# Performance work log

Hardware: AMD Instinct MI355X
Metric: run time of the kernel (lower is better)

Reference implementation:

```python
import jax, jax.numpy as jnp
import numpy as np
from jax import lax

# ---- fixed configuration (matches init_kwargs / input_specs) ----
L, E, V, F, HU, HL, S = 32, 1024, 2048, 8, 128, 2, 7
D0, D1R, D1E = 512, 129, 640
D = S + 1                      # path dimension = num_slices + 1
SIGLEN = D + D * D + D * D * D # iisignature.siglength(8, 3) = 584
FINAL = F * 2 * SIGLEN         # 9344
EPS = 1e-5                     # BatchNorm eps


def _bn(x, g, b):
    # BatchNorm1d in training mode: biased batch statistics over axis 0
    mu = x.mean(0)
    var = x.var(0)
    return (x - mu) / jnp.sqrt(var + EPS) * g + b


def _mlp(x, Win, bin_, gin, betain, Wh, bh, gh, betah, Wout, bout, gout, betaout):
    # eigf: Linear+BN+ReLU blocks, 1 -> HU -> ... -> HU -> 1
    h = jax.nn.relu(_bn(x @ Win.T + bin_, gin, betain))
    for l in range(HL):
        h = jax.nn.relu(_bn(h @ Wh[l].T + bh[l], gh[l], betah[l]))
    o = jax.nn.relu(_bn(h @ Wout.T + bout, gout, betaout))
    return o[:, 0]


# ---- path signature, level 3, via Chen's identity (replaces iisignature.sig) ----
def _seg(dx):
    s1 = dx
    s2 = jnp.outer(s1, dx).reshape(-1) * 0.5
    s3 = jnp.outer(s2, dx).reshape(-1) / 3.0
    return (s1, s2, s3)


def _chen(Sg, T):
    s1, s2, s3 = Sg
    t1, t2, t3 = T
    r1 = s1 + t1
    r2 = s2 + t2 + jnp.outer(s1, t1).reshape(-1)
    r3 = s3 + t3 + jnp.outer(s1, t2).reshape(-1) + jnp.outer(s2, t1).reshape(-1)
    return (r1, r2, r3)


def _sig3(path):  # path [P, D] -> [SIGLEN]
    dX = path[1:] - path[:-1]

    def step(Sg, dx):
        return _chen(Sg, _seg(dx)), None

    Sg, _ = lax.scan(step, _seg(dX[0]), dX[1:])
    return jnp.concatenate(Sg)


def _diagram_sig(vals, W_proj, b_proj):
    # Conv1d(1, S, kernel=2, stride=2) == pairwise projection; then sort, prepend time axis
    pairs = vals.reshape(-1, 2)                      # [P, 2]
    P = pairs.shape[0]
    proj = jnp.einsum('pk,sk->sp', pairs, W_proj[:, 0, :]) + b_proj[:, None]  # [S, P]
    proj = jnp.sort(proj, axis=-1)
    t = jnp.arange(P, dtype=vals.dtype) / (P * (P + 1) / 2.0)
    path = jnp.concatenate([t[None, :], proj], axis=0).T  # [P, D]
    return _sig3(path)


def setup_inputs() -> dict:
    key = jax.random.key(0)
    ks = iter(jax.random.split(key, 16))
    nrm = lambda kk, shp, sc: jax.random.normal(kk, shp, jnp.float32) * sc
    inp = {
        "eigenvalues": jax.random.uniform(next(ks), (L, E), jnp.float32),
        "eigenvectors_sq": jax.random.uniform(next(ks), (L, E, V), jnp.float32) / E,
        "dgm0": jax.random.randint(next(ks), (L, F, D0), 0, V, jnp.int32),
        "dgm1rel": jax.random.randint(next(ks), (L, F, D1R), 0, V, jnp.int32),
        "dgm1ext": jax.random.randint(next(ks), (L, F, D1E), 0, V, jnp.int32),
        "mlp_Win": nrm(next(ks), (F, HU, 1), 1.0),
        "mlp_bin": jnp.zeros((F, HU), jnp.float32),
        "mlp_gin": jnp.ones((F, HU), jnp.float32),
        "mlp_betain": jnp.zeros((F, HU), jnp.float32),
        "mlp_Wh": nrm(next(ks), (F, HL, HU, HU), 1.0 / np.sqrt(HU)),
        "mlp_bh": jnp.zeros((F, HL, HU), jnp.float32),
        "mlp_gh": jnp.ones((F, HL, HU), jnp.float32),
        "mlp_betah": jnp.zeros((F, HL, HU), jnp.float32),
        "mlp_Wout": nrm(next(ks), (F, 1, HU), 1.0 / np.sqrt(HU)),
        "mlp_bout": jnp.zeros((F, 1), jnp.float32),
        "mlp_gout": jnp.ones((F, 1), jnp.float32),
        "mlp_betaout": jnp.zeros((F, 1), jnp.float32),
        "W_proj": nrm(next(ks), (S, 1, 2), 0.7),
        "b_proj": jnp.zeros((S,), jnp.float32),
        "W_fin": nrm(next(ks), (1, FINAL), 1.0 / np.sqrt(FINAL)),
        "b_fin": jnp.zeros((1,), jnp.float32),
        "g_fin": jnp.ones((1,), jnp.float32),
        "beta_fin": jnp.zeros((1,), jnp.float32),
    }
    return inp


def reference(eigenvalues, eigenvectors_sq, dgm0, dgm1rel, dgm1ext,
              mlp_Win, mlp_bin, mlp_gin, mlp_betain,
              mlp_Wh, mlp_bh, mlp_gh, mlp_betah,
              mlp_Wout, mlp_bout, mlp_gout, mlp_betaout,
              W_proj, b_proj, W_fin, b_fin, g_fin, beta_fin):
    flat = eigenvalues.reshape(-1, 1)  # [L*E, 1], sample-major like the torch flatten
    evs = jax.vmap(lambda *p: _mlp(flat, *p))(
        mlp_Win, mlp_bin, mlp_gin, mlp_betain,
        mlp_Wh, mlp_bh, mlp_gh, mlp_betah,
        mlp_Wout, mlp_bout, mlp_gout, mlp_betaout)  # [F, L*E]
    # per-sample filtration values: evs_transformed[:, slice_i] @ eigvecsq_i
    f = jnp.einsum('fle,lev->lfv', evs.reshape(F, L, E), eigenvectors_sq)  # [L, F, V]
    fv = f.reshape(L * F, V)
    d0 = jnp.take_along_axis(fv, dgm0.reshape(L * F, D0), axis=1)
    rel = jnp.take_along_axis(fv, dgm1rel.reshape(L * F, D1R), axis=1)
    # torch.arange(len-1, 0, -1): reversed, dropping element 0
    Dgm0 = jnp.concatenate([d0, rel[:, 1:][:, ::-1]], axis=1)  # [L*F, 640]
    Dgm1 = jnp.take_along_axis(fv, dgm1ext.reshape(L * F, D1E), axis=1)
    sig0 = jax.vmap(lambda v: _diagram_sig(v, W_proj, b_proj))(Dgm0)  # [L*F, SIGLEN]
    sig1 = jax.vmap(lambda v: _diagram_sig(v, W_proj, b_proj))(Dgm1)
    x = jnp.concatenate([sig0, sig1], axis=-1).reshape(L, FINAL)
    out = x @ W_fin.T + b_fin  # dropout p=0.0 -> identity
    return _bn(out, g_fin, beta_fin)  # [L, 1]
```

## Files before the change

kernel.cpp:

```cpp
#include <hip/hip_runtime.h>
#include <cfloat>
#include <math.h>

#define N_SAMP 32768
#define FF 8
#define HU 128
#define LL 32
#define EE 1024
#define VV 2048
#define PP 320
#define SIGLEN 584
#define FINAL_W 9344

__device__ __forceinline__ int frag_pos(int m) {
  return ((m & 4) << 4) | ((m >> 3) << 2) | (m & 3);
}

__device__ __forceinline__ double wave_red(double v) {
#pragma unroll
  for (int off = 32; off > 0; off >>= 1) v += __shfl_xor(v, off, 64);
  return v;
}

__global__ __launch_bounds__(256) void k_xstats(const float* __restrict__ x,
                                                double* __restrict__ xst) {
  const int tid = threadIdx.x;
  double s1 = 0.0, s2 = 0.0;
  for (int i = tid; i < N_SAMP; i += 256) { double v = (double)x[i]; s1 += v; s2 += v * v; }
  __shared__ double r1[4], r2[4];
  double w1 = wave_red(s1), w2 = wave_red(s2);
  int wave = tid >> 6, lane = tid & 63;
  if (lane == 0) { r1[wave] = w1; r2[wave] = w2; }
  __syncthreads();
  if (tid == 0) {
    xst[0] = r1[0] + r1[1] + r1[2] + r1[3];
    xst[1] = r2[0] + r2[1] + r2[2] + r2[3];
  }
}

template<int MODE>
__global__ __launch_bounds__(256, 4)
void k_gemm(const float* __restrict__ Ain,
            const double* __restrict__ xstats,
            const float* __restrict__ w_in,
            const float* __restrict__ g_in,
            const float* __restrict__ beta_in,
            const float* __restrict__ sc,
            const float* __restrict__ sh,
            const float* __restrict__ Wb, int wstride,
            const float* __restrict__ bb, int bstride,
            float* __restrict__ Yt_out,
            double* __restrict__ stats) {
  __shared__ __align__(16) float As[32][132];
  __shared__ __align__(16) float Bs[32][132];
  __shared__ __align__(16) float p0[HU], p1[HU], biasl[HU], xl[HU];
  const int tid = threadIdx.x;
  const int f = blockIdx.y;
  const int m0 = blockIdx.x * 128;

  if (tid < HU) {
    biasl[tid] = bb[(size_t)f * bstride + tid];
    if (MODE == 0) {
      double mx = xstats[0] * (1.0 / 32768.0);
      double vx = xstats[1] * (1.0 / 32768.0) - mx * mx;
      if (vx < 0) vx = 0;
      float w = w_in[f * HU + tid];
      double inv = 1.0 / sqrt((double)w * (double)w * vx + 1e-5);
      float sj = (float)inv * g_in[f * HU + tid] * w;
      p0[tid] = sj;
      p1[tid] = beta_in[f * HU + tid] - (float)mx * sj;
      xl[tid] = Ain[m0 + tid];
    } else {
      p0[tid] = sc[f * HU + tid];
      p1[tid] = sh[f * HU + tid];
    }
  }

  float cacc[8][8];
#pragma unroll
  for (int i = 0; i < 8; ++i)
#pragma unroll
    for (int j = 0; j < 8; ++j) cacc[i][j] = 0.f;

  const int tidm = tid & 15, tidn = tid >> 4;

  for (int kk = 0; kk < 128; kk += 32) {
    __syncthreads();
#pragma unroll
    for (int r = 0; r < 4; ++r) {
      int flat4 = tid + r * 256;
      int k = flat4 >> 5;
      int mc = flat4 & 31;
      int pos = ((mc & 1) << 6) | ((mc >> 1) << 2);
      float a0, a1, a2, a3;
      if (MODE == 0) {
        const float4 xv = *(const float4*)&xl[mc * 4];
        float s = p0[kk + k], t = p1[kk + k];
        a0 = fmaxf(fmaf(xv.x, s, t), 0.f);
        a1 = fmaxf(fmaf(xv.y, s, t), 0.f);
        a2 = fmaxf(fmaf(xv.z, s, t), 0.f);
        a3 = fmaxf(fmaf(xv.w, s, t), 0.f);
      } else {
        const float4 yv = *(const float4*)(Ain + ((size_t)(f * HU + kk + k)) * N_SAMP + m0 + mc * 4);
        float s = p0[kk + k], t = p1[kk + k];
        a0 = fmaxf(fmaf(yv.x, s, t), 0.f);
        a1 = fmaxf(fmaf(yv.y, s, t), 0.f);
        a2 = fmaxf(fmaf(yv.z, s, t), 0.f);
        a3 = fmaxf(fmaf(yv.w, s, t), 0.f);
      }
      *(float4*)&As[k][pos] = make_float4(a0, a1, a2, a3);
    }
#pragma unroll
    for (int r = 0; r < 4; ++r) {
      int flat = tid + r * 256;
      int n = flat >> 3, kf = flat & 7;
      const float4 wv = *(const float4*)(Wb + (size_t)f * wstride + n * HU + kk + kf * 4);
      int pn = frag_pos(n);
      Bs[kf * 4 + 0][pn] = wv.x;
      Bs[kf * 4 + 1][pn] = wv.y;
      Bs[kf * 4 + 2][pn] = wv.z;
      Bs[kf * 4 + 3][pn] = wv.w;
    }
    __syncthreads();
#pragma unroll
    for (int k = 0; k < 32; ++k) {
      float4 a0 = *(const float4*)&As[k][tidm * 4];
      float4 a1 = *(const float4*)&As[k][64 + tidm * 4];
      float4 b0 = *(const float4*)&Bs[k][tidn * 4];
      float4 b1 = *(const float4*)&Bs[k][64 + tidn * 4];
      float av[8] = {a0.x, a0.y, a0.z, a0.w, a1.x, a1.y, a1.z, a1.w};
      float bv[8] = {b0.x, b0.y, b0.z, b0.w, b1.x, b1.y, b1.z, b1.w};
#pragma unroll
      for (int i = 0; i < 8; ++i)
#pragma unroll
        for (int j = 0; j < 8; ++j) cacc[i][j] = fmaf(av[i], bv[j], cacc[i][j]);
    }
  }
  __syncthreads();

  float cs1[8], cs2[8];
#pragma unroll
  for (int j = 0; j < 8; ++j) { cs1[j] = 0.f; cs2[j] = 0.f; }
#pragma unroll
  for (int jj = 0; jj < 8; ++jj) {
    int j = tidn * 8 + jj;
    float b = biasl[j];
    float o[8];
#pragma unroll
    for (int i = 0; i < 8; ++i) {
      float v = cacc[i][jj] + b;
      o[i] = v;
      cs1[jj] += v;
      cs2[jj] = fmaf(v, v, cs2[jj]);
    }
    float* dst = Yt_out + ((size_t)(f * HU + j)) * N_SAMP + m0 + tidm * 8;
    *(float4*)dst = make_float4(o[0], o[1], o[2], o[3]);
    *(float4*)(dst + 4) = make_float4(o[4], o[5], o[6], o[7]);
  }
  float* red1 = &As[0][0];
  float* red2 = &Bs[0][0];
#pragma unroll
  for (int j = 0; j < 8; ++j) red1[tidm * 128 + tidn * 8 + j] = cs1[j];
#pragma unroll
  for (int j = 0; j < 8; ++j) red2[tidm * 128 + tidn * 8 + j] = cs2[j];
  __syncthreads();
  {
    int which = tid >> 7, n = tid & 127;
    const float* rp = which ? red2 : red1;
    float s = 0.f;
#pragma unroll
    for (int r = 0; r < 16; ++r) s += rp[r * 128 + n];
    atomicAdd(&stats[(f * HU + n) * 2 + which], (double)s);
  }
}

__global__ __launch_bounds__(256) void k_fin(const double* __restrict__ stats,
                                             const float* __restrict__ g,
                                             const float* __restrict__ beta,
                                             int per_f, int gstride, int count,
                                             float* __restrict__ sc, float* __restrict__ sh) {
  int idx = blockIdx.x * 256 + threadIdx.x;
  if (idx >= count) return;
  int f = idx / per_f, j = idx - f * per_f;
  double S1 = stats[idx * 2 + 0], S2 = stats[idx * 2 + 1];
  double mean = S1 * (1.0 / 32768.0);
  double var = S2 * (1.0 / 32768.0) - mean * mean;
  if (var < 0) var = 0;
  double inv = 1.0 / sqrt(var + 1e-5);
  float gg = g[f * gstride + j];
  float scv = (float)inv * gg;
  sc[idx] = scv;
  sh[idx] = beta[f * gstride + j] - (float)mean * scv;
}

__global__ __launch_bounds__(256, 4) void k_outlayer(const float* __restrict__ Yt,
                                                     const float* __restrict__ sc2,
                                                     const float* __restrict__ sh2,
                                                     const float* __restrict__ Wout,
                                                     const float* __restrict__ bout,
                                                     float* __restrict__ evs_pre,
                                                     double* __restrict__ stats3) {
  __shared__ float wj[HU], scl[HU], shl[HU];
  const int tid = threadIdx.x;
  const int f = blockIdx.y;
  const int i = blockIdx.x * 256 + tid;
  if (tid < HU) {
    wj[tid] = Wout[f * HU + tid];
    scl[tid] = sc2[f * HU + tid];
    shl[tid] = sh2[f * HU + tid];
  }
  __syncthreads();
  const float* base = Yt + (size_t)f * HU * N_SAMP + i;
  float acc = 0.f;
#pragma unroll
  for (int j = 0; j < HU; ++j) {
    float y = base[(size_t)j * N_SAMP];
    acc = fmaf(fmaxf(fmaf(y, scl[j], shl[j]), 0.f), wj[j], acc);
  }
  float yo = acc + bout[f];
  evs_pre[(size_t)f * N_SAMP + i] = yo;
  double v = (double)yo;
  double s1 = wave_red(v), s2 = wave_red(v * v);
  __shared__ double r1[4], r2[4];
  int wave = tid >> 6, lane = tid & 63;
  if (lane == 0) { r1[wave] = s1; r2[wave] = s2; }
  __syncthreads();
  if (tid == 0) atomicAdd(&stats3[f * 2 + 0], r1[0] + r1[1] + r1[2] + r1[3]);
  if (tid == 1) atomicAdd(&stats3[f * 2 + 1], r2[0] + r2[1] + r2[2] + r2[3]);
}

__global__ __launch_bounds__(256) void k_einsum(const float* __restrict__ evs_pre,
                                                const float* __restrict__ sc3,
                                                const float* __restrict__ sh3,
                                                const float* __restrict__ eig,
                                                float* __restrict__ fv) {
  __shared__ float ev[FF * EE];
  const int tid = threadIdx.x;
  const int l = blockIdx.y;
  const int v0 = blockIdx.x * 256;
#pragma unroll
  for (int r = 0; r < 32; ++r) {
    int q = tid + r * 256;
    int f = q >> 10, e = q & 1023;
    float y = evs_pre[(size_t)f * N_SAMP + l * EE + e];
    ev[q] = fmaxf(fmaf(y, sc3[f], sh3[f]), 0.f);
  }
  __syncthreads();
  const float* up = eig + (size_t)l * EE * VV + v0 + tid;
  float acc[8] = {0, 0, 0, 0, 0, 0, 0, 0};
  for (int e0 = 0; e0 < EE; e0 += 32) {
    float u[32];
#pragma unroll
    for (int t = 0; t < 32; ++t) u[t] = up[(size_t)(e0 + t) * VV];
#pragma unroll
    for (int t = 0; t < 32; ++t) {
#pragma unroll
      for (int f = 0; f < 8; ++f) acc[f] = fmaf(ev[f * EE + e0 + t], u[t], acc[f]);
    }
  }
#pragma unroll
  for (int f = 0; f < 8; ++f) fv[((size_t)(l * FF + f)) * VV + v0 + tid] = acc[f];
}

__global__ __launch_bounds__(256) void k_diagram(const float* __restrict__ fv,
                                                 const int* __restrict__ dgm0,
                                                 const int* __restrict__ dgm1rel,
                                                 const int* __restrict__ dgm1ext,
                                                 const float* __restrict__ Wp,
                                                 const float* __restrict__ bp,
                                                 float* __restrict__ xbuf) {
  __shared__ float vals[640];
  __shared__ float ps[7 * 512];
  __shared__ float dXl[320][8];
  const int tid = threadIdx.x;
  const int bid = blockIdx.x;
  const int row = bid >> 1;
  const int c = bid & 1;
  const float* fvr = fv + (size_t)row * VV;

  for (int k = tid; k < 640; k += 256) {
    int idx;
    if (c == 0) idx = (k < 512) ? dgm0[(size_t)row * 512 + k] : dgm1rel[(size_t)row * 129 + (640 - k)];
    else        idx = dgm1ext[(size_t)row * 640 + k];
    vals[k] = fvr[idx];
  }
  __syncthreads();
  for (int q = tid; q < 7 * 512; q += 256) {
    int s = q >> 9, p = q & 511;
    float pv = 3.402823466e+38f;
    if (p < PP) pv = fmaf(Wp[2 * s + 1], vals[2 * p + 1], fmaf(Wp[2 * s], vals[2 * p], bp[s]));
    ps[s * 512 + p] = pv;
  }
  for (int k = 2; k <= 512; k <<= 1) {
    for (int j = k >> 1; j > 0; j >>= 1) {
      __syncthreads();
      for (int q = tid; q < 1792; q += 256) {
        int s = q >> 8, ip = q & 255;
        int i = ((ip & ~(j - 1)) << 1) | (ip & (j - 1));
        int p2 = i | j;
        float a = ps[s * 512 + i], b = ps[s * 512 + p2];
        bool up = ((i & k) == 0);
        if ((a > b) == up) { ps[s * 512 + i] = b; ps[s * 512 + p2] = a; }
      }
    }
  }
  __syncthreads();
  for (int q = tid; q < 319 * 8; q += 256) {
    int p = q >> 3, d = q & 7;
    dXl[p][d] = (d == 0) ? (1.0f / 51360.0f)
                         : ps[(d - 1) * 512 + p + 1] - ps[(d - 1) * 512 + p];
  }
  __syncthreads();
  if (tid < 64) {
    const int a = tid >> 3, b = tid & 7;
    float s1a = 0.f, s2r = 0.f;
    float s3r[8] = {0, 0, 0, 0, 0, 0, 0, 0};
    for (int p = 0; p < 319; ++p) {
      float4 dlo = *(const float4*)&dXl[p][0];
      float4 dhi = *(const float4*)&dXl[p][4];
      float dxa = dXl[p][a];
      float dxb = dXl[p][b];
      float coefA = fmaf(dxa, (1.f / 3.f), s1a);
      float w = fmaf(0.5f * dxb, coefA, s2r);
      s2r = fmaf(dxb, fmaf(0.5f, dxa, s1a), s2r);
      s3r[0] = fmaf(w, dlo.x, s3r[0]);
      s3r[1] = fmaf(w, dlo.y, s3r[1]);
      s3r[2] = fmaf(w, dlo.z, s3r[2]);
      s3r[3] = fmaf(w, dlo.w, s3r[3]);
      s3r[4] = fmaf(w, dhi.x, s3r[4]);
      s3r[5] = fmaf(w, dhi.y, s3r[5]);
      s3r[6] = fmaf(w, dhi.z, s3r[6]);
      s3r[7] = fmaf(w, dhi.w, s3r[7]);
      s1a += dxa;
    }
    const int l = row >> 3, ff = row & 7;
    float* xr = xbuf + (size_t)l * FINAL_W + ff * (2 * SIGLEN) + c * SIGLEN;
    if ((tid & 7) == 0) xr[a] = s1a;
    xr[8 + tid] = s2r;
    float* s3p = xr + 72 + tid * 8;
    *(float4*)(s3p + 0) = make_float4(s3r[0], s3r[1], s3r[2], s3r[3]);
    *(float4*)(s3p + 4) = make_float4(s3r[4], s3r[5], s3r[6], s3r[7]);
  }
}

__global__ __launch_bounds__(256) void k_rowdot(const float* __restrict__ xbuf,
                                                const float* __restrict__ Wf,
                                                const float* __restrict__ bf,
                                                double* __restrict__ outpre) {
  const int tid = threadIdx.x, l = blockIdx.x;
  const float* xr = xbuf + (size_t)l * FINAL_W;
  double acc = 0.0;
  for (int k = tid; k < FINAL_W; k += 256) acc += (double)xr[k] * (double)Wf[k];
  acc = wave_red(acc);
  __shared__ double r[4];
  int wave = tid >> 6, lane = tid & 63;
  if (lane == 0) r[wave] = acc;
  __syncthreads();
  if (tid == 0) outpre[l] = r[0] + r[1] + r[2] + r[3] + (double)bf[0];
}

__global__ __launch_bounds__(64) void k_bnfin(const double* __restrict__ outpre,
                                              const float* __restrict__ g,
                                              const float* __restrict__ beta,
                                              float* __restrict__ dout) {
  int i = threadIdx.x;
  double v = (i < 32) ? outpre[i] : 0.0;
  double s1 = wave_red(v);
  double s2 = wave_red(v * v);
  double mean = s1 * (1.0 / 32.0);
  double var = s2 * (1.0 / 32.0) - mean * mean;
  if (var < 0) var = 0;
  double inv = 1.0 / sqrt(var + 1e-5);
  if (i < 32) dout[i] = (float)((v - mean) * inv * (double)g[0] + (double)beta[0]);
}

extern "C" void kernel_launch(void* const* d_in, const int* in_sizes, int n_in,
                              void* d_out, int out_size, void* d_ws, size_t ws_size,
                              hipStream_t stream) {
  const float* eig     = (const float*)d_in[0];
  const float* eigsq   = (const float*)d_in[1];
  const int*   dgm0    = (const int*)d_in[2];
  const int*   dgm1rel = (const int*)d_in[3];
  const int*   dgm1ext = (const int*)d_in[4];
  const float* Win     = (const float*)d_in[5];
  const float* gin     = (const float*)d_in[7];
  const float* betain  = (const float*)d_in[8];
  const float* Wh      = (const float*)d_in[9];
  const float* bh      = (const float*)d_in[10];
  const float* gh      = (const float*)d_in[11];
  const float* betah   = (const float*)d_in[12];
  const float* Wout    = (const float*)d_in[13];
  const float* bout    = (const float*)d_in[14];
  const float* gout    = (const float*)d_in[15];
  const float* betaout = (const float*)d_in[16];
  const float* Wp      = (const float*)d_in[17];
  const float* bp      = (const float*)d_in[18];
  const float* Wfin    = (const float*)d_in[19];
  const float* bfin    = (const float*)d_in[20];
  const float* gfin    = (const float*)d_in[21];
  const float* betafin = (const float*)d_in[22];

  char* ws = (char*)d_ws;
  float*  Yt      = (float*)(ws);
  float*  evs_pre = (float*)(ws + 134217728u);
  float*  fv      = (float*)(ws + 135266304u);
  float*  xbuf    = (float*)(ws + 137363456u);
  float*  sc1     = (float*)(ws + 138559488u);
  float*  sh1     = sc1 + 1024;
  float*  sc2     = sc1 + 2048;
  float*  sh2     = sc1 + 3072;
  float*  sc3     = sc1 + 4096;
  float*  sh3     = sc1 + 4160;
  double* stats1  = (double*)(ws + 138576384u);
  double* stats2  = stats1 + 2048;
  double* stats3  = stats1 + 4096;
  double* xstats  = stats1 + 4112;
  double* outpre  = stats1 + 4114;

  hipMemsetAsync(stats1, 0, 4114 * sizeof(double), stream);

  k_xstats<<<1, 256, 0, stream>>>(eig, xstats);
  k_gemm<0><<<dim3(256, FF), 256, 0, stream>>>(eig, xstats, Win, gin, betain,
                                               nullptr, nullptr,
                                               Wh, 32768, bh, 256, Yt, stats1);
  k_fin<<<4, 256, 0, stream>>>(stats1, gh, betah, 128, 256, 1024, sc1, sh1);
  k_gemm<1><<<dim3(256, FF), 256, 0, stream>>>(Yt, nullptr, nullptr, nullptr, nullptr,
                                               sc1, sh1,
                                               Wh + 16384, 32768, bh + 128, 256, Yt, stats2);
  k_fin<<<4, 256, 0, stream>>>(stats2, gh + 128, betah + 128, 128, 256, 1024, sc2, sh2);
  k_outlayer<<<dim3(128, FF), 256, 0, stream>>>(Yt, sc2, sh2, Wout, bout, evs_pre, stats3);
  k_fin<<<1, 256, 0, stream>>>(stats3, gout, betaout, 1, 1, 8, sc3, sh3);
  k_einsum<<<dim3(8, 32), 256, 0, stream>>>(evs_pre, sc3, sh3, eigsq, fv);
  k_diagram<<<512, 256, 0, stream>>>(fv, dgm0, dgm1rel, dgm1ext, Wp, bp, xbuf);
  k_rowdot<<<32, 256, 0, stream>>>(xbuf, Wfin, bfin, outpre);
  k_bnfin<<<1, 64, 0, stream>>>(outpre, gfin, betafin, (float*)d_out);
}
```

Baseline: 806.2 us.

## Run hidden-layer GEMMs on bf16 MFMA with three-way split emulating fp32

Replaces the scalar-FMA fp32 tiled GEMM for the two hidden MLP layers with a matrix-core kernel. Each fp32 operand is split into three bf16 parts (hi/mid/lo) and six cross-term MFMAs are accumulated to keep near-fp32 accuracy. Weights are pre-split by a new small kernel, and activations are split on the fly while staging into shared memory. This aims to cut ALU-bound GEMM time, at the cost of more shared memory, lower occupancy, extra split work, and a small loss of precision from the dropped cross terms.

```diff
diff --git a/kernel.cpp b/kernel.cpp
--- a/kernel.cpp
+++ b/kernel.cpp
@@ -5,21 +5,46 @@
 #define N_SAMP 32768
 #define FF 8
 #define HU 128
-#define LL 32
 #define EE 1024
 #define VV 2048
 #define PP 320
 #define SIGLEN 584
 #define FINAL_W 9344
 
-__device__ __forceinline__ int frag_pos(int m) {
-  return ((m & 4) << 4) | ((m >> 3) << 2) | (m & 3);
+typedef unsigned short u16;
+typedef unsigned int u32;
+typedef short s16x8 __attribute__((ext_vector_type(8)));
+typedef float f32x4 __attribute__((ext_vector_type(4)));
+
+__device__ __forceinline__ u16 f2bf(float v) {
+  u32 u = __float_as_uint(v);
+  return (u16)((u + 0x7fffu + ((u >> 16) & 1u)) >> 16);
+}
+__device__ __forceinline__ float bf2f(u16 h) {
+  return __uint_as_float(((u32)h) << 16);
+}
+__device__ __forceinline__ void split3(float v, u16& h, u16& m, u16& l) {
+  h = f2bf(v);
+  float r = v - bf2f(h);
+  m = f2bf(r);
+  float r2 = r - bf2f(m);
+  l = f2bf(r2);
 }
 
 __device__ __forceinline__ double wave_red(double v) {
 #pragma unroll
   for (int off = 32; off > 0; off >>= 1) v += __shfl_xor(v, off, 64);
   return v;
+}
+
+__global__ __launch_bounds__(256) void k_wsplit(const float* __restrict__ W,
+                                                u16* __restrict__ Hh, u16* __restrict__ Hm,
+                                                u16* __restrict__ Hl, int n) {
+  int i = blockIdx.x * 256 + threadIdx.x;
+  if (i >= n) return;
+  u16 h, m, l;
+  split3(W[i], h, m, l);
+  Hh[i] = h; Hm[i] = m; Hl[i] = l;
 }
 
 __global__ __launch_bounds__(256) void k_xstats(const float* __restrict__ x,
@@ -39,24 +64,29 @@
 }
 
 template<int MODE>
-__global__ __launch_bounds__(256, 4)
-void k_gemm(const float* __restrict__ Ain,
-            const double* __restrict__ xstats,
-            const float* __restrict__ w_in,
-            const float* __restrict__ g_in,
-            const float* __restrict__ beta_in,
-            const float* __restrict__ sc,
-            const float* __restrict__ sh,
-            const float* __restrict__ Wb, int wstride,
-            const float* __restrict__ bb, int bstride,
-            float* __restrict__ Yt_out,
-            double* __restrict__ stats) {
-  __shared__ __align__(16) float As[32][132];
-  __shared__ __align__(16) float Bs[32][132];
-  __shared__ __align__(16) float p0[HU], p1[HU], biasl[HU], xl[HU];
+__global__ __launch_bounds__(256, 2)
+void k_mgemm(const float* __restrict__ Ain,
+             const double* __restrict__ xstats,
+             const float* __restrict__ w_in,
+             const float* __restrict__ g_in,
+             const float* __restrict__ beta_in,
+             const float* __restrict__ sc,
+             const float* __restrict__ sh,
+             const u16* __restrict__ Wh_,
+             const u16* __restrict__ Wm_,
+             const u16* __restrict__ Wl_,
+             const float* __restrict__ bb, int bstride,
+             float* __restrict__ Yt_out,
+             double* __restrict__ stats) {
+  __shared__ u16 SB[6][128 * 40];
+  __shared__ float p0[HU], p1[HU], biasl[HU], xl[HU];
+  u16* Ah = SB[0]; u16* Am = SB[1]; u16* Al = SB[2];
+  u16* Bh = SB[3]; u16* Bm = SB[4]; u16* Bl = SB[5];
+
   const int tid = threadIdx.x;
   const int f = blockIdx.y;
   const int m0 = blockIdx.x * 128;
+  const int lane = tid & 63, ln = tid & 15, quad = (tid >> 4) & 3, wave = tid >> 6;
 
   if (tid < HU) {
     biasl[tid] = bb[(size_t)f * bstride + tid];
@@ -76,93 +106,130 @@
     }
   }
 
-  float cacc[8][8];
-#pragma unroll
-  for (int i = 0; i < 8; ++i)
-#pragma unroll
-    for (int j = 0; j < 8; ++j) cacc[i][j] = 0.f;
-
-  const int tidm = tid & 15, tidn = tid >> 4;
+  f32x4 acc[2][8];
+#pragma unroll
+  for (int mt = 0; mt < 2; ++mt)
+#pragma unroll
+    for (int u = 0; u < 8; ++u) acc[mt][u] = (f32x4){0.f, 0.f, 0.f, 0.f};
+
+  __syncthreads();
 
   for (int kk = 0; kk < 128; kk += 32) {
+    if (MODE == 0) {
+      const int m = tid >> 1, kh = (tid & 1) * 16;
+      const float xv = xl[m];
+      u32 ph[8], pm[8], pl[8];
+#pragma unroll
+      for (int jp = 0; jp < 8; ++jp) {
+        u16 h0, m_0, l0, h1, m_1, l1;
+        int k = kh + jp * 2;
+        split3(fmaxf(fmaf(xv, p0[kk + k], p1[kk + k]), 0.f), h0, m_0, l0);
+        split3(fmaxf(fmaf(xv, p0[kk + k + 1], p1[kk + k + 1]), 0.f), h1, m_1, l1);
+        ph[jp] = (u32)h0 | ((u32)h1 << 16);
+        pm[jp] = (u32)m_0 | ((u32)m_1 << 16);
+        pl[jp] = (u32)l0 | ((u32)l1 << 16);
+      }
+      int off = m * 40 + kh;
+      *(uint4*)&Ah[off] = make_uint4(ph[0], ph[1], ph[2], ph[3]);
+      *(uint4*)&Ah[off + 8] = make_uint4(ph[4], ph[5], ph[6], ph[7]);
+      *(uint4*)&Am[off] = make_uint4(pm[0], pm[1], pm[2], pm[3]);
+      *(uint4*)&Am[off + 8] = make_uint4(pm[4], pm[5], pm[6], pm[7]);
+      *(uint4*)&Al[off] = make_uint4(pl[0], pl[1], pl[2], pl[3]);
+      *(uint4*)&Al[off + 8] = make_uint4(pl[4], pl[5], pl[6], pl[7]);
+    } else {
+#pragma unroll
+      for (int r = 0; r < 4; ++r) {
+        int flat = tid + r * 256;
+        int m = flat & 127, kq = flat >> 7;
+        const float* src = Ain + ((size_t)(f * HU + kk + kq * 4)) * N_SAMP + m0 + m;
+        u32 ph[2], pm[2], pl[2];
+#pragma unroll
+        for (int ip = 0; ip < 2; ++ip) {
+          int k = kq * 4 + ip * 2;
+          float v0 = fmaxf(fmaf(src[(size_t)(ip * 2) * N_SAMP], p0[kk + k], p1[kk + k]), 0.f);
+          float v1 = fmaxf(fmaf(src[(size_t)(ip * 2 + 1) * N_SAMP], p0[kk + k + 1], p1[kk + k + 1]), 0.f);
+          u16 h0, m_0, l0, h1, m_1, l1;
+          split3(v0, h0, m_0, l0);
+          split3(v1, h1, m_1, l1);
+          ph[ip] = (u32)h0 | ((u32)h1 << 16);
+          pm[ip] = (u32)m_0 | ((u32)m_1 << 16);
+          pl[ip] = (u32)l0 | ((u32)l1 << 16);
+        }
+        int off = m * 40 + kq * 4;
+        *(uint2*)&Ah[off] = make_uint2(ph[0], ph[1]);
+        *(uint2*)&Am[off] = make_uint2(pm[0], pm[1]);
+        *(uint2*)&Al[off] = make_uint2(pl[0], pl[1]);
+      }
+    }
+#pragma unroll
+    for (int r = 0; r < 2; ++r) {
+      int flat = tid + r * 256;
+      int n = flat >> 2, c = flat & 3;
+      size_t g = (size_t)f * (2 * HU * HU) + (size_t)n * HU + kk + c * 8;
+      int off = n * 40 + c * 8;
+      *(uint4*)&Bh[off] = *(const uint4*)&Wh_[g];
+      *(uint4*)&Bm[off] = *(const uint4*)&Wm_[g];
+      *(uint4*)&Bl[off] = *(const uint4*)&Wl_[g];
+    }
     __syncthreads();
-#pragma unroll
-    for (int r = 0; r < 4; ++r) {
-      int flat4 = tid + r * 256;
-      int k = flat4 >> 5;
-      int mc = flat4 & 31;
-      int pos = ((mc & 1) << 6) | ((mc >> 1) << 2);
-      float a0, a1, a2, a3;
-      if (MODE == 0) {
-        const float4 xv = *(const float4*)&xl[mc * 4];
-        float s = p0[kk + k], t = p1[kk + k];
-        a0 = fmaxf(fmaf(xv.x, s, t), 0.f);
-        a1 = fmaxf(fmaf(xv.y, s, t), 0.f);
-        a2 = fmaxf(fmaf(xv.z, s, t), 0.f);
-        a3 = fmaxf(fmaf(xv.w, s, t), 0.f);
-      } else {
-        const float4 yv = *(const float4*)(Ain + ((size_t)(f * HU + kk + k)) * N_SAMP + m0 + mc * 4);
-        float s = p0[kk + k], t = p1[kk + k];
-        a0 = fmaxf(fmaf(yv.x, s, t), 0.f);
-        a1 = fmaxf(fmaf(yv.y, s, t), 0.f);
-        a2 = fmaxf(fmaf(yv.z, s, t), 0.f);
-        a3 = fmaxf(fmaf(yv.w, s, t), 0.f);
+    s16x8 af0[3], af1[3];
+    {
+      int r0 = (wave * 32 + ln) * 40 + quad * 8;
+      int r1 = (wave * 32 + 16 + ln) * 40 + quad * 8;
+      af0[0] = *(const s16x8*)&Ah[r0]; af0[1] = *(const s16x8*)&Am[r0]; af0[2] = *(const s16x8*)&Al[r0];
+      af1[0] = *(const s16x8*)&Ah[r1]; af1[1] = *(const s16x8*)&Am[r1]; af1[2] = *(const s16x8*)&Al[r1];
+    }
+#pragma unroll
+    for (int u = 0; u < 8; ++u) {
+      int bo = (u * 16 + ln) * 40 + quad * 8;
+      s16x8 bh = *(const s16x8*)&Bh[bo];
+      s16x8 bm = *(const s16x8*)&Bm[bo];
+      s16x8 bl = *(const s16x8*)&Bl[bo];
+      f32x4 a0 = acc[0][u], a1 = acc[1][u];
+      a0 = __builtin_amdgcn_mfma_f32_16x16x32_bf16(af0[0], bh, a0, 0, 0, 0);
+      a1 = __builtin_amdgcn_mfma_f32_16x16x32_bf16(af1[0], bh, a1, 0, 0, 0);
+      a0 = __builtin_amdgcn_mfma_f32_16x16x32_bf16(af0[1], bh, a0, 0, 0, 0);
+      a1 = __builtin_amdgcn_mfma_f32_16x16x32_bf16(af1[1], bh, a1, 0, 0, 0);
+      a0 = __builtin_amdgcn_mfma_f32_16x16x32_bf16(af0[0], bm, a0, 0, 0, 0);
+      a1 = __builtin_amdgcn_mfma_f32_16x16x32_bf16(af1[0], bm, a1, 0, 0, 0);
+      a0 = __builtin_amdgcn_mfma_f32_16x16x32_bf16(af0[2], bh, a0, 0, 0, 0);
+      a1 = __builtin_amdgcn_mfma_f32_16x16x32_bf16(af1[2], bh, a1, 0, 0, 0);
+      a0 = __builtin_amdgcn_mfma_f32_16x16x32_bf16(af0[1], bm, a0, 0, 0, 0);
+      a1 = __builtin_amdgcn_mfma_f32_16x16x32_bf16(af1[1], bm, a1, 0, 0, 0);
+      a0 = __builtin_amdgcn_mfma_f32_16x16x32_bf16(af0[0], bl, a0, 0, 0, 0);
+      a1 = __builtin_amdgcn_mfma_f32_16x16x32_bf16(af1[0], bl, a1, 0, 0, 0);
+      acc[0][u] = a0; acc[1][u] = a1;
+    }
+    __syncthreads();
+  }
+
+  float cs1[8], cs2[8];
+#pragma unroll
+  for (int u = 0; u < 8; ++u) { cs1[u] = 0.f; cs2[u] = 0.f; }
+#pragma unroll
+  for (int u = 0; u < 8; ++u) {
+    float b = biasl[u * 16 + ln];
+#pragma unroll
+    for (int mt = 0; mt < 2; ++mt) {
+#pragma unroll
+      for (int reg = 0; reg < 4; ++reg) {
+        float v = acc[mt][u][reg] + b;
+        acc[mt][u][reg] = v;
+        cs1[u] += v;
+        cs2[u] = fmaf(v, v, cs2[u]);
       }
-      *(float4*)&As[k][pos] = make_float4(a0, a1, a2, a3);
-    }
-#pragma unroll
-    for (int r = 0; r < 4; ++r) {
-      int flat = tid + r * 256;
-      int n = flat >> 3, kf = flat & 7;
-      const float4 wv = *(const float4*)(Wb + (size_t)f * wstride + n * HU + kk + kf * 4);
-      int pn = frag_pos(n);
-      Bs[kf * 4 + 0][pn] = wv.x;
-      Bs[kf * 4 + 1][pn] = wv.y;
-      Bs[kf * 4 + 2][pn] = wv.z;
-      Bs[kf * 4 + 3][pn] = wv.w;
-    }
-    __syncthreads();
-#pragma unroll
-    for (int k = 0; k < 32; ++k) {
-      float4 a0 = *(const float4*)&As[k][tidm * 4];
-      float4 a1 = *(const float4*)&As[k][64 + tidm * 4];
-      float4 b0 = *(const float4*)&Bs[k][tidn * 4];
-      float4 b1 = *(const float4*)&Bs[k][64 + tidn * 4];
-      float av[8] = {a0.x, a0.y, a0.z, a0.w, a1.x, a1.y, a1.z, a1.w};
-      float bv[8] = {b0.x, b0.y, b0.z, b0.w, b1.x, b1.y, b1.z, b1.w};
-#pragma unroll
-      for (int i = 0; i < 8; ++i)
-#pragma unroll
-        for (int j = 0; j < 8; ++j) cacc[i][j] = fmaf(av[i], bv[j], cacc[i][j]);
-    }
-  }
-  __syncthreads();
-
-  float cs1[8], cs2[8];
-#pragma unroll
-  for (int j = 0; j < 8; ++j) { cs1[j] = 0.f; cs2[j] = 0.f; }
-#pragma unroll
-  for (int jj = 0; jj < 8; ++jj) {
-    int j = tidn * 8 + jj;
-    float b = biasl[j];
-    float o[8];
-#pragma unroll
-    for (int i = 0; i < 8; ++i) {
-      float v = cacc[i][jj] + b;
-      o[i] = v;
-      cs1[jj] += v;
-      cs2[jj] = fmaf(v, v, cs2[jj]);
-    }
-    float* dst = Yt_out + ((size_t)(f * HU + j)) * N_SAMP + m0 + tidm * 8;
-    *(float4*)dst = make_float4(o[0], o[1], o[2], o[3]);
-    *(float4*)(dst + 4) = make_float4(o[4], o[5], o[6], o[7]);
-  }
-  float* red1 = &As[0][0];
-  float* red2 = &Bs[0][0];
-#pragma unroll
-  for (int j = 0; j < 8; ++j) red1[tidm * 128 + tidn * 8 + j] = cs1[j];
-#pragma unroll
-  for (int j = 0; j < 8; ++j) red2[tidm * 128 + tidn * 8 + j] = cs2[j];
+      float4 st = make_float4(acc[mt][u][0], acc[mt][u][1], acc[mt][u][2], acc[mt][u][3]);
+      *(float4*)&Yt_out[((size_t)(f * HU + u * 16 + ln)) * N_SAMP + m0 + wave * 32 + mt * 16 + quad * 4] = st;
+    }
+  }
+  float* red1 = (float*)&SB[0][0];
+  float* red2 = red1 + 2048;
+  int wq = wave * 4 + quad;
+#pragma unroll
+  for (int u = 0; u < 8; ++u) {
+    red1[wq * 128 + u * 16 + ln] = cs1[u];
+    red2[wq * 128 + u * 16 + ln] = cs2[u];
+  }
   __syncthreads();
   {
     int which = tid >> 7, n = tid & 127;
@@ -416,17 +483,23 @@
   double* stats3  = stats1 + 4096;
   double* xstats  = stats1 + 4112;
   double* outpre  = stats1 + 4114;
+  u16*    Whh     = (u16*)(ws + 138612736u);
+  u16*    Whm     = (u16*)(ws + 139137024u);
+  u16*    Whl     = (u16*)(ws + 139661312u);
 
   hipMemsetAsync(stats1, 0, 4114 * sizeof(double), stream);
 
+  k_wsplit<<<1024, 256, 0, stream>>>(Wh, Whh, Whm, Whl, FF * 2 * HU * HU);
   k_xstats<<<1, 256, 0, stream>>>(eig, xstats);
-  k_gemm<0><<<dim3(256, FF), 256, 0, stream>>>(eig, xstats, Win, gin, betain,
-                                               nullptr, nullptr,
-                                               Wh, 32768, bh, 256, Yt, stats1);
+  k_mgemm<0><<<dim3(256, FF), 256, 0, stream>>>(eig, xstats, Win, gin, betain,
+                                                nullptr, nullptr,
+                                                Whh, Whm, Whl,
+                                                bh, 256, Yt, stats1);
   k_fin<<<4, 256, 0, stream>>>(stats1, gh, betah, 128, 256, 1024, sc1, sh1);
-  k_gemm<1><<<dim3(256, FF), 256, 0, stream>>>(Yt, nullptr, nullptr, nullptr, nullptr,
-                                               sc1, sh1,
-                                               Wh + 16384, 32768, bh + 128, 256, Yt, stats2);
+  k_mgemm<1><<<dim3(256, FF), 256, 0, stream>>>(Yt, nullptr, nullptr, nullptr, nullptr,
+                                                sc1, sh1,
+                                                Whh + HU * HU, Whm + HU * HU, Whl + HU * HU,
+                                                bh + 128, 256, Yt, stats2);
   k_fin<<<4, 256, 0, stream>>>(stats2, gh + 128, betah + 128, 128, 256, 1024, sc2, sh2);
   k_outlayer<<<dim3(128, FF), 256, 0, stream>>>(Yt, sc2, sh2, Wout, bout, evs_pre, stats3);
   k_fin<<<1, 256, 0, stream>>>(stats3, gout, betaout, 1, 1, 8, sc3, sh3);
```

After: 743.8 us. -7.7%, faster.
